# Kernel tuning notes

Measured on AMD Instinct MI355X. Metric: run time of the kernel, lower is better.

The kernel has to match this reference:

```python
import jax, jax.numpy as jnp
import numpy as np


def setup_inputs() -> dict:
    key = jax.random.key(0)
    ks = jax.random.split(key, 5)
    d_out, d_in = 4096, 4096
    r = min(d_out, d_in)
    B, T = 4, 2048
    x = jax.random.normal(ks[0], (B, T, d_in), dtype=jnp.float32)
    U = jax.random.normal(ks[1], (d_out, r), dtype=jnp.float32)
    S = jax.random.uniform(ks[2], (r,), dtype=jnp.float32)
    Vt = jax.random.normal(ks[3], (r, d_in), dtype=jnp.float32)
    epsilon = jnp.zeros((r,), dtype=jnp.float32)
    bias = jax.random.normal(ks[4], (d_out,), dtype=jnp.float32)
    return {"x": x, "U": U, "S": S, "Vt": Vt, "epsilon": epsilon, "bias": bias}


def reference(x, U, S, Vt, epsilon, bias):
    # w = U @ diag(S + epsilon) @ Vt  (diag folded as column scale of U)
    w = (U * (S + epsilon)[None, :]) @ Vt  # [d_out, d_in]
    # F.linear: y = x @ w.T + bias
    return jnp.einsum('btk,ok->bto', x, w) + bias
```

## Files before the change

### kernel.cpp

```cpp
#include <hip/hip_runtime.h>
#include <hip/hip_bf16.h>
#include <stdint.h>

typedef __attribute__((ext_vector_type(4))) float f32x4;
typedef __attribute__((ext_vector_type(8))) short short8v;

typedef __attribute__((address_space(1))) void gvoid;
typedef __attribute__((address_space(3))) void lvoid;

#define GLD16(gp, lp) __builtin_amdgcn_global_load_lds((const gvoid*)(gp), (lvoid*)(lp), 16, 0, 0)

__device__ __forceinline__ unsigned short f2bf(float f) {
    union { float ff; unsigned uu; } a; a.ff = f;
    unsigned u = a.uu;
    u += 0x7FFFu + ((u >> 16) & 1u);
    return (unsigned short)(u >> 16);
}

__global__ __launch_bounds__(256) void prep_fused_kernel(
    const float* __restrict__ U, const float* __restrict__ S,
    const float* __restrict__ eps, unsigned short* __restrict__ Ub,
    const float* __restrict__ Vt, unsigned short* __restrict__ VtT) {
    __shared__ float tile[64][65];
    if (blockIdx.x < 8192) {
        long idx = ((long)blockIdx.x * 256 + threadIdx.x) * 8;
        int r = (int)(idx & 4095);
        f32x4 u0 = *(const f32x4*)(U + idx);
        f32x4 u1 = *(const f32x4*)(U + idx + 4);
        f32x4 s0 = *(const f32x4*)(S + r);
        f32x4 s1 = *(const f32x4*)(S + r + 4);
        f32x4 e0 = *(const f32x4*)(eps + r);
        f32x4 e1 = *(const f32x4*)(eps + r + 4);
        union { uint4 v; unsigned short s[8]; } o;
#pragma unroll
        for (int j = 0; j < 4; ++j) {
            o.s[j]     = f2bf(u0[j] * (s0[j] + e0[j]));
            o.s[j + 4] = f2bf(u1[j] * (s1[j] + e1[j]));
        }
        *(uint4*)(Ub + idx) = o.v;
    } else {
        int t  = blockIdx.x - 8192;
        int k0 = (t & 63) << 6;
        int r0 = (t >> 6) << 6;
        int tx = threadIdx.x & 63;
        int tq = threadIdx.x >> 6;
#pragma unroll
        for (int i = 0; i < 16; ++i) {
            int row = (i << 2) + tq;
            tile[row][tx] = Vt[(long)(r0 + row) * 4096 + k0 + tx];
        }
        __syncthreads();
#pragma unroll
        for (int i = 0; i < 16; ++i) {
            int krow = (i << 2) + tq;
            VtT[(long)(k0 + krow) * 4096 + r0 + tx] = f2bf(tile[tx][krow]);
        }
    }
}

__global__ __launch_bounds__(256) void cvt_bf16_kernel(
    const float* __restrict__ src, unsigned short* __restrict__ dst) {
    long idx = ((long)blockIdx.x * 256 + threadIdx.x) * 8;
    f32x4 v0 = *(const f32x4*)(src + idx);
    f32x4 v1 = *(const f32x4*)(src + idx + 4);
    union { uint4 v; unsigned short s[8]; } o;
#pragma unroll
    for (int j = 0; j < 4; ++j) {
        o.s[j]     = f2bf(v0[j]);
        o.s[j + 4] = f2bf(v1[j]);
    }
    *(uint4*)(dst + idx) = o.v;
}

#define MM(a, b, c) __builtin_amdgcn_mfma_f32_16x16x32_bf16(a, b, c, 0, 0, 0)

#define ARG(r) (As + (r) * 8192)
#define BRG(r) (Bs + (r) * 8192)

#define STAGE_A(r, koff) do { \
    const unsigned short* _s = A + gAr + (koff); \
    unsigned short* _d = ARG(r) + wave * 512; \
    GLD16(_s, _d); GLD16(_s + (long)128 * K, _d + 4096); } while (0)

#define STAGE_B(r, koff) do { \
    const unsigned short* _s = B + gBr + (koff); \
    unsigned short* _d = BRG(r) + wave * 512; \
    GLD16(_s, _d); GLD16(_s + (long)128 * K, _d + 4096); } while (0)

#define DSR(dst, base, imm) \
    asm volatile("ds_read_b128 %0, %1 offset:%c2" \
                 : "=v"(dst) : "v"(base), "i"(imm))

#define READ_AB(bk, R) do { \
    DSR(aB[bk][0][0], aByte, (R)*16384 + 0);            \
    DSR(aB[bk][0][1], aByte, (R)*16384 + 1024);         \
    DSR(aB[bk][0][2], aByte, (R)*16384 + 2048);         \
    DSR(aB[bk][0][3], aByte, (R)*16384 + 3072);         \
    DSR(aB[bk][1][0], aByte, (R)*16384 + 4096);         \
    DSR(aB[bk][1][1], aByte, (R)*16384 + 5120);         \
    DSR(aB[bk][1][2], aByte, (R)*16384 + 6144);         \
    DSR(aB[bk][1][3], aByte, (R)*16384 + 7168);         \
    DSR(bB[bk][0],    bByte, (R)*16384 + 0);            \
    DSR(bB[bk][1],    bByte, (R)*16384 + 1024);         \
    DSR(bB[bk][2],    bByte, (R)*16384 + 2048);         \
    DSR(bB[bk][3],    bByte, (R)*16384 + 3072); } while (0)

#define MFMA32(bk) do { \
    _Pragma("unroll") \
    for (int _h = 0; _h < 2; ++_h) \
    _Pragma("unroll") \
    for (int _m = 0; _m < 4; ++_m) { \
        acc[_h*4+_m][0] = MM(aB[bk][_h][_m], bB[bk][0], acc[_h*4+_m][0]); \
        acc[_h*4+_m][1] = MM(aB[bk][_h][_m], bB[bk][1], acc[_h*4+_m][1]); \
        acc[_h*4+_m][2] = MM(aB[bk][_h][_m], bB[bk][2], acc[_h*4+_m][2]); \
        acc[_h*4+_m][3] = MM(aB[bk][_h][_m], bB[bk][3], acc[_h*4+_m][3]); \
    } } while (0)

#define SGB __builtin_amdgcn_sched_group_barrier

#define PHASE(rN, sb, rS, sk, cb) do { \
    STAGE_A(rS, sk); STAGE_B(rS, sk); \
    asm volatile("s_waitcnt lgkmcnt(0)" ::: "memory"); \
    __builtin_amdgcn_sched_barrier(0); \
    __builtin_amdgcn_s_setprio(1); \
    READ_AB(sb, rN); \
    MFMA32(cb); \
    _Pragma("unroll") \
    for (int _g = 0; _g < 12; ++_g) { SGB(0x008, 2, 0); SGB(0x100, 1, 0); } \
    SGB(0x008, 8, 0); \
    __builtin_amdgcn_s_setprio(0); \
    asm volatile("s_waitcnt vmcnt(4)" ::: "memory"); \
    __builtin_amdgcn_s_barrier(); } while (0)

template<int OUT_BF16, int BIAS>
__global__ __launch_bounds__(512, 2) void gemm256_kernel(
    const unsigned short* __restrict__ A,
    const unsigned short* __restrict__ B,
    void* __restrict__ Cv, const float* __restrict__ bias,
    int M, int N, int K) {
    __shared__ unsigned short As[4 * 8192];
    __shared__ unsigned short Bs[4 * 8192];

    const int tid  = threadIdx.x;
    const int wave = tid >> 6;
    const int lane = tid & 63;
    const int fr   = lane & 15;
    const int fq   = lane >> 4;

    const int nwg = gridDim.x;
    const int bid = blockIdx.x;
    const int cpx = nwg >> 3;
    const int wg  = (bid & 7) * cpx + (bid >> 3);
    const int nmt = M >> 8;
    const long n0 = (long)(2 * (wg / cpx) + (wg & 1)) << 8;
    const long m0 = (long)((wg >> 1) & (nmt - 1)) << 8;

    const int wwr = wave >> 2;
    const int wwc = wave & 3;

    const int  rS  = tid >> 2;
    const int  sS  = (tid & 3) ^ ((rS >> 1) & 3);
    const long gAr = (m0 + rS) * K + sS * 8;
    const long gBr = (n0 + rS) * K + sS * 8;

    const int swz   = (fq ^ ((fr >> 1) & 3)) * 8;
    const int aBase = (wwr * 128 + fr) * 32 + swz;
    const int bBase = (wwc * 64 + fr) * 32 + swz;
    const unsigned aByte = (unsigned)(uintptr_t)(As + aBase);
    const unsigned bByte = (unsigned)(uintptr_t)(Bs + bBase);

    f32x4  acc[8][4] = {};
    short8v aB[2][2][4], bB[2][4];

    STAGE_A(0, 0);  STAGE_B(0, 0);
    STAGE_A(1, 32); STAGE_B(1, 32);
    STAGE_A(2, 64); STAGE_B(2, 64);
    asm volatile("s_waitcnt vmcnt(4)" ::: "memory");
    __builtin_amdgcn_s_barrier();
    READ_AB(0, 0);

    const int nIter = K >> 7;
    for (int i = 0; i < nIter; ++i) {
        const int kA = 128 * i + 96;
        int k0n = 128 * i + 128; if (k0n >= K) k0n -= K;
        int k1n = 128 * i + 160; if (k1n >= K) k1n -= K;
        int k2n = 128 * i + 192; if (k2n >= K) k2n -= K;

        PHASE(1, 1, 3, kA,  0);
        PHASE(2, 0, 0, k0n, 1);
        PHASE(3, 1, 1, k1n, 0);
        PHASE(0, 0, 2, k2n, 1);
    }

#pragma unroll
    for (int nf = 0; nf < 4; ++nf) {
        const int col = (int)n0 + wwc * 64 + nf * 16 + fr;
        float bv = BIAS ? bias[col] : 0.0f;
#pragma unroll
        for (int mf = 0; mf < 8; ++mf) {
            f32x4 v = acc[mf][nf];
            long rowb = m0 + wwr * 128 + mf * 16 + fq * 4;
#pragma unroll
            for (int j = 0; j < 4; ++j) {
                float val = v[j] + bv;
                long off = (rowb + j) * N + col;
                if (OUT_BF16) ((unsigned short*)Cv)[off] = f2bf(val);
                else          ((float*)Cv)[off] = val;
            }
        }
    }
}

extern "C" void kernel_launch(void* const* d_in, const int* in_sizes, int n_in,
                              void* d_out, int out_size, void* d_ws, size_t ws_size,
                              hipStream_t stream) {
    const float* x    = (const float*)d_in[0];
    const float* U    = (const float*)d_in[1];
    const float* S    = (const float*)d_in[2];
    const float* Vt   = (const float*)d_in[3];
    const float* eps  = (const float*)d_in[4];
    const float* bias = (const float*)d_in[5];
    float* out = (float*)d_out;

    char* ws = (char*)d_ws;
    unsigned short* Ub  = (unsigned short*)(ws);
    unsigned short* VtT = (unsigned short*)(ws + (size_t)(32 << 20));
    unsigned short* Wb  = (unsigned short*)(ws + (size_t)(64 << 20));
    unsigned short* Xb  = (unsigned short*)(ws);

    prep_fused_kernel<<<12288, 256, 0, stream>>>(U, S, eps, Ub, Vt, VtT);
    gemm256_kernel<1, 0><<<256, 512, 0, stream>>>(Ub, VtT, (void*)Wb, nullptr,
                                                  4096, 4096, 4096);
    cvt_bf16_kernel<<<16384, 256, 0, stream>>>(x, Xb);
    gemm256_kernel<0, 1><<<512, 512, 0, stream>>>(Xb, Wb, (void*)out, bias,
                                                  8192, 4096, 4096);
}
```

Measured before the change: 433.6 us.

## Fuse x fp32-to-bf16 conversion into the weight-building GEMM main loop

Removes the separate conversion kernel for x and instead has each thread of the first GEMM load and convert a chunk of x once per K iteration. The conversion loads are interleaved with the LDS staging, with adjusted vmcnt waits, so they can hide behind MFMA work. This saves a kernel launch and lets the bandwidth-bound conversion overlap the compute-bound GEMM. In exchange it needs a larger workspace (falling back to the old path otherwise) and adds register and memory pressure to the GEMM pipeline.

```diff
diff --git a/kernel.cpp b/kernel.cpp
--- a/kernel.cpp
+++ b/kernel.cpp
@@ -118,6 +118,11 @@
 
 #define SGB __builtin_amdgcn_sched_group_barrier
 
+#define SGB_PATTERN do { \
+    _Pragma("unroll") \
+    for (int _g = 0; _g < 12; ++_g) { SGB(0x008, 2, 0); SGB(0x100, 1, 0); } \
+    SGB(0x008, 8, 0); } while (0)
+
 #define PHASE(rN, sb, rS, sk, cb) do { \
     STAGE_A(rS, sk); STAGE_B(rS, sk); \
     asm volatile("s_waitcnt lgkmcnt(0)" ::: "memory"); \
@@ -125,18 +130,26 @@
     __builtin_amdgcn_s_setprio(1); \
     READ_AB(sb, rN); \
     MFMA32(cb); \
-    _Pragma("unroll") \
-    for (int _g = 0; _g < 12; ++_g) { SGB(0x008, 2, 0); SGB(0x100, 1, 0); } \
-    SGB(0x008, 8, 0); \
+    SGB_PATTERN; \
     __builtin_amdgcn_s_setprio(0); \
     asm volatile("s_waitcnt vmcnt(4)" ::: "memory"); \
     __builtin_amdgcn_s_barrier(); } while (0)
 
-template<int OUT_BF16, int BIAS>
+#define XCVT_STORE do { \
+    union { uint4 v; unsigned short s[8]; } _o; \
+    _Pragma("unroll") \
+    for (int _j = 0; _j < 4; ++_j) { \
+        _o.s[_j]     = f2bf(xv0[_j]); \
+        _o.s[_j + 4] = f2bf(xv1[_j]); } \
+    *reinterpret_cast<uint4*>((uintptr_t)xsaddr) = _o.v; \
+    xsaddr += 2097152ull; } while (0)
+
+template<int OUT_BF16, int BIAS, int DO_CVT>
 __global__ __launch_bounds__(512, 2) void gemm256_kernel(
     const unsigned short* __restrict__ A,
     const unsigned short* __restrict__ B,
     void* __restrict__ Cv, const float* __restrict__ bias,
+    const float* __restrict__ xsrc, unsigned short* __restrict__ xdst,
     int M, int N, int K) {
     __shared__ unsigned short As[4 * 8192];
     __shared__ unsigned short Bs[4 * 8192];
@@ -172,6 +185,14 @@
     f32x4  acc[8][4] = {};
     short8v aB[2][2][4], bB[2][4];
 
+    f32x4 xv0, xv1;
+    unsigned long long xaddr = 0, xsaddr = 0;
+    if constexpr (DO_CVT) {
+        long gchunk = ((long)bid * 512 + tid);
+        xaddr  = (unsigned long long)(uintptr_t)(xsrc + gchunk * 8);
+        xsaddr = (unsigned long long)(uintptr_t)(xdst + gchunk * 8);
+    }
+
     STAGE_A(0, 0);  STAGE_B(0, 0);
     STAGE_A(1, 32); STAGE_B(1, 32);
     STAGE_A(2, 64); STAGE_B(2, 64);
@@ -186,11 +207,32 @@
         int k1n = 128 * i + 160; if (k1n >= K) k1n -= K;
         int k2n = 128 * i + 192; if (k2n >= K) k2n -= K;
 
-        PHASE(1, 1, 3, kA,  0);
+        if constexpr (DO_CVT) {
+            if (i) XCVT_STORE;
+            asm volatile("global_load_dwordx4 %0, %2, off\n\t"
+                         "global_load_dwordx4 %1, %2, off offset:16"
+                         : "=&v"(xv0), "=&v"(xv1) : "v"(xaddr));
+            xaddr += 4194304ull;
+            STAGE_A(3, kA); STAGE_B(3, kA);
+            asm volatile("s_waitcnt lgkmcnt(0)" ::: "memory");
+            __builtin_amdgcn_sched_barrier(0);
+            __builtin_amdgcn_s_setprio(1);
+            READ_AB(1, 1);
+            MFMA32(0);
+            SGB_PATTERN;
+            __builtin_amdgcn_s_setprio(0);
+            if (i) asm volatile("s_waitcnt vmcnt(7)" ::: "memory");
+            else   asm volatile("s_waitcnt vmcnt(6)" ::: "memory");
+            __builtin_amdgcn_s_barrier();
+        } else {
+            PHASE(1, 1, 3, kA,  0);
+        }
         PHASE(2, 0, 0, k0n, 1);
         PHASE(3, 1, 1, k1n, 0);
         PHASE(0, 0, 2, k2n, 1);
     }
+
+    if constexpr (DO_CVT) XCVT_STORE;
 
 #pragma unroll
     for (int nf = 0; nf < 4; ++nf) {
@@ -226,12 +268,21 @@
     unsigned short* Ub  = (unsigned short*)(ws);
     unsigned short* VtT = (unsigned short*)(ws + (size_t)(32 << 20));
     unsigned short* Wb  = (unsigned short*)(ws + (size_t)(64 << 20));
-    unsigned short* Xb  = (unsigned short*)(ws);
 
     prep_fused_kernel<<<12288, 256, 0, stream>>>(U, S, eps, Ub, Vt, VtT);
-    gemm256_kernel<1, 0><<<256, 512, 0, stream>>>(Ub, VtT, (void*)Wb, nullptr,
-                                                  4096, 4096, 4096);
-    cvt_bf16_kernel<<<16384, 256, 0, stream>>>(x, Xb);
-    gemm256_kernel<0, 1><<<512, 512, 0, stream>>>(Xb, Wb, (void*)out, bias,
-                                                  8192, 4096, 4096);
-}
+
+    if (ws_size >= ((size_t)160 << 20)) {
+        unsigned short* Xb = (unsigned short*)(ws + ((size_t)96 << 20));
+        gemm256_kernel<1, 0, 1><<<256, 512, 0, stream>>>(
+            Ub, VtT, (void*)Wb, nullptr, x, Xb, 4096, 4096, 4096);
+        gemm256_kernel<0, 1, 0><<<512, 512, 0, stream>>>(
+            Xb, Wb, (void*)out, bias, nullptr, nullptr, 8192, 4096, 4096);
+    } else {
+        unsigned short* Xb = (unsigned short*)(ws);
+        gemm256_kernel<1, 0, 0><<<256, 512, 0, stream>>>(
+            Ub, VtT, (void*)Wb, nullptr, nullptr, nullptr, 4096, 4096, 4096);
+        cvt_bf16_kernel<<<16384, 256, 0, stream>>>(x, Xb);
+        gemm256_kernel<0, 1, 0><<<512, 512, 0, stream>>>(
+            Xb, Wb, (void*)out, bias, nullptr, nullptr, 8192, 4096, 4096);
+    }
+}
```

After: 428.3 us (median of 3 runs). No clear change (-1.2%).

## Use 1024-thread GEMM tiles and fuse x bf16 conversion into first GEMM

Applied to the files above, without the earlier changes.

Moves the GEMM to 16 waves per 256x256 tile, so each wave computes 64x64 and holds 16 accumulators instead of 32. It drops the hand-scheduled double-buffered ds_read/MFMA interleave in favour of plain LDS loads and a simpler vmcnt(2) wait per phase. When the workspace is large enough, the first GEMM also converts x to bf16 inside its main loop, hiding the separate conversion kernel's memory traffic behind the W computation. The risks are losing the tuned instruction schedule and losing register-level reuse with smaller per-wave tiles.

```diff
diff --git a/kernel.cpp b/kernel.cpp
--- a/kernel.cpp
+++ b/kernel.cpp
@@ -77,66 +77,45 @@
 #define ARG(r) (As + (r) * 8192)
 #define BRG(r) (Bs + (r) * 8192)
 
-#define STAGE_A(r, koff) do { \
-    const unsigned short* _s = A + gAr + (koff); \
-    unsigned short* _d = ARG(r) + wave * 512; \
-    GLD16(_s, _d); GLD16(_s + (long)128 * K, _d + 4096); } while (0)
-
-#define STAGE_B(r, koff) do { \
-    const unsigned short* _s = B + gBr + (koff); \
-    unsigned short* _d = BRG(r) + wave * 512; \
-    GLD16(_s, _d); GLD16(_s + (long)128 * K, _d + 4096); } while (0)
-
-#define DSR(dst, base, imm) \
-    asm volatile("ds_read_b128 %0, %1 offset:%c2" \
-                 : "=v"(dst) : "v"(base), "i"(imm))
-
-#define READ_AB(bk, R) do { \
-    DSR(aB[bk][0][0], aByte, (R)*16384 + 0);            \
-    DSR(aB[bk][0][1], aByte, (R)*16384 + 1024);         \
-    DSR(aB[bk][0][2], aByte, (R)*16384 + 2048);         \
-    DSR(aB[bk][0][3], aByte, (R)*16384 + 3072);         \
-    DSR(aB[bk][1][0], aByte, (R)*16384 + 4096);         \
-    DSR(aB[bk][1][1], aByte, (R)*16384 + 5120);         \
-    DSR(aB[bk][1][2], aByte, (R)*16384 + 6144);         \
-    DSR(aB[bk][1][3], aByte, (R)*16384 + 7168);         \
-    DSR(bB[bk][0],    bByte, (R)*16384 + 0);            \
-    DSR(bB[bk][1],    bByte, (R)*16384 + 1024);         \
-    DSR(bB[bk][2],    bByte, (R)*16384 + 2048);         \
-    DSR(bB[bk][3],    bByte, (R)*16384 + 3072); } while (0)
-
-#define MFMA32(bk) do { \
+#define STAGE_A(r, koff) GLD16(A + gAr + (koff), ARG(r) + wave * 512)
+#define STAGE_B(r, koff) GLD16(B + gBr + (koff), BRG(r) + wave * 512)
+
+#define LOAD_A(r) do { \
+    const unsigned short* _p = ARG(r) + aBase; \
     _Pragma("unroll") \
-    for (int _h = 0; _h < 2; ++_h) \
+    for (int _m = 0; _m < 4; ++_m) aR[_m] = *(const short8v*)(_p + _m * 512); } while (0)
+
+#define READ_B(r) do { \
+    const unsigned short* _p = BRG(r) + bBase; \
+    _Pragma("unroll") \
+    for (int _n = 0; _n < 4; ++_n) bR[_n] = *(const short8v*)(_p + _n * 512); } while (0)
+
+#define MFMA16 do { \
+    __builtin_amdgcn_s_setprio(1); \
     _Pragma("unroll") \
     for (int _m = 0; _m < 4; ++_m) { \
-        acc[_h*4+_m][0] = MM(aB[bk][_h][_m], bB[bk][0], acc[_h*4+_m][0]); \
-        acc[_h*4+_m][1] = MM(aB[bk][_h][_m], bB[bk][1], acc[_h*4+_m][1]); \
-        acc[_h*4+_m][2] = MM(aB[bk][_h][_m], bB[bk][2], acc[_h*4+_m][2]); \
-        acc[_h*4+_m][3] = MM(aB[bk][_h][_m], bB[bk][3], acc[_h*4+_m][3]); \
-    } } while (0)
-
-#define SGB __builtin_amdgcn_sched_group_barrier
-
-#define PHASE(rN, sb, rS, sk, cb) do { \
-    STAGE_A(rS, sk); STAGE_B(rS, sk); \
-    asm volatile("s_waitcnt lgkmcnt(0)" ::: "memory"); \
-    __builtin_amdgcn_sched_barrier(0); \
-    __builtin_amdgcn_s_setprio(1); \
-    READ_AB(sb, rN); \
-    MFMA32(cb); \
-    _Pragma("unroll") \
-    for (int _g = 0; _g < 12; ++_g) { SGB(0x008, 2, 0); SGB(0x100, 1, 0); } \
-    SGB(0x008, 8, 0); \
-    __builtin_amdgcn_s_setprio(0); \
-    asm volatile("s_waitcnt vmcnt(4)" ::: "memory"); \
-    __builtin_amdgcn_s_barrier(); } while (0)
-
-template<int OUT_BF16, int BIAS>
-__global__ __launch_bounds__(512, 2) void gemm256_kernel(
+        acc[_m][0] = MM(aR[_m], bR[0], acc[_m][0]); \
+        acc[_m][1] = MM(aR[_m], bR[1], acc[_m][1]); \
+        acc[_m][2] = MM(aR[_m], bR[2], acc[_m][2]); \
+        acc[_m][3] = MM(aR[_m], bR[3], acc[_m][3]); \
+    } \
+    __builtin_amdgcn_s_setprio(0); } while (0)
+
+#define VM2 asm volatile("s_waitcnt vmcnt(2)" ::: "memory")
+#define BAR __builtin_amdgcn_s_barrier()
+
+#define PHASE(rd, st, sk) do { \
+    LOAD_A(rd); READ_B(rd); \
+    STAGE_A(st, sk); STAGE_B(st, sk); \
+    MFMA16; \
+    VM2; BAR; } while (0)
+
+template<int OUT_BF16, int BIAS, int DO_CVT>
+__global__ __launch_bounds__(1024, 4) void gemm256_kernel(
     const unsigned short* __restrict__ A,
     const unsigned short* __restrict__ B,
     void* __restrict__ Cv, const float* __restrict__ bias,
+    const float* __restrict__ xsrc, unsigned short* __restrict__ xdst,
     int M, int N, int K) {
     __shared__ unsigned short As[4 * 8192];
     __shared__ unsigned short Bs[4 * 8192];
@@ -164,20 +143,26 @@
     const long gBr = (n0 + rS) * K + sS * 8;
 
     const int swz   = (fq ^ ((fr >> 1) & 3)) * 8;
-    const int aBase = (wwr * 128 + fr) * 32 + swz;
+    const int aBase = (wwr * 64 + fr) * 32 + swz;
     const int bBase = (wwc * 64 + fr) * 32 + swz;
-    const unsigned aByte = (unsigned)(uintptr_t)(As + aBase);
-    const unsigned bByte = (unsigned)(uintptr_t)(Bs + bBase);
-
-    f32x4  acc[8][4] = {};
-    short8v aB[2][2][4], bB[2][4];
+
+    f32x4  acc[4][4] = {};
+    short8v aR[4], bR[4];
+
+    f32x4 xv;
+    unsigned long long xaddr = 0;
+    unsigned short* xs = nullptr;
+    if constexpr (DO_CVT) {
+        long base = (long)bid * 4096 + (long)tid * 4;
+        xaddr = (unsigned long long)(uintptr_t)(xsrc + base);
+        xs = xdst + base;
+    }
 
     STAGE_A(0, 0);  STAGE_B(0, 0);
     STAGE_A(1, 32); STAGE_B(1, 32);
     STAGE_A(2, 64); STAGE_B(2, 64);
-    asm volatile("s_waitcnt vmcnt(4)" ::: "memory");
-    __builtin_amdgcn_s_barrier();
-    READ_AB(0, 0);
+    VM2;
+    BAR;
 
     const int nIter = K >> 7;
     for (int i = 0; i < nIter; ++i) {
@@ -186,10 +171,34 @@
         int k1n = 128 * i + 160; if (k1n >= K) k1n -= K;
         int k2n = 128 * i + 192; if (k2n >= K) k2n -= K;
 
-        PHASE(1, 1, 3, kA,  0);
-        PHASE(2, 0, 0, k0n, 1);
-        PHASE(3, 1, 1, k1n, 0);
-        PHASE(0, 0, 2, k2n, 1);
+        if constexpr (DO_CVT) {
+            LOAD_A(0); READ_B(0);
+            if (i) {
+                union { unsigned uu[2]; unsigned short s[4]; } o;
+#pragma unroll
+                for (int j = 0; j < 4; ++j) o.s[j] = f2bf(xv[j]);
+                *(uint2*)xs = *(uint2*)o.uu;
+                xs += 1048576;
+            }
+            asm volatile("global_load_dwordx4 %0, %1, off"
+                         : "=v"(xv) : "v"(xaddr));
+            xaddr += 4194304ull;
+            STAGE_A(3, kA); STAGE_B(3, kA);
+            MFMA16;
+            VM2; BAR;
+        } else {
+            PHASE(0, 3, kA);
+        }
+        PHASE(1, 0, k0n);
+        PHASE(2, 1, k1n);
+        PHASE(3, 2, k2n);
+    }
+
+    if constexpr (DO_CVT) {
+        union { unsigned uu[2]; unsigned short s[4]; } o;
+#pragma unroll
+        for (int j = 0; j < 4; ++j) o.s[j] = f2bf(xv[j]);
+        *(uint2*)xs = *(uint2*)o.uu;
     }
 
 #pragma unroll
@@ -197,9 +206,9 @@
         const int col = (int)n0 + wwc * 64 + nf * 16 + fr;
         float bv = BIAS ? bias[col] : 0.0f;
 #pragma unroll
-        for (int mf = 0; mf < 8; ++mf) {
+        for (int mf = 0; mf < 4; ++mf) {
             f32x4 v = acc[mf][nf];
-            long rowb = m0 + wwr * 128 + mf * 16 + fq * 4;
+            long rowb = m0 + wwr * 64 + mf * 16 + fq * 4;
 #pragma unroll
             for (int j = 0; j < 4; ++j) {
                 float val = v[j] + bv;
@@ -226,12 +235,21 @@
     unsigned short* Ub  = (unsigned short*)(ws);
     unsigned short* VtT = (unsigned short*)(ws + (size_t)(32 << 20));
     unsigned short* Wb  = (unsigned short*)(ws + (size_t)(64 << 20));
-    unsigned short* Xb  = (unsigned short*)(ws);
 
     prep_fused_kernel<<<12288, 256, 0, stream>>>(U, S, eps, Ub, Vt, VtT);
-    gemm256_kernel<1, 0><<<256, 512, 0, stream>>>(Ub, VtT, (void*)Wb, nullptr,
-                                                  4096, 4096, 4096);
-    cvt_bf16_kernel<<<16384, 256, 0, stream>>>(x, Xb);
-    gemm256_kernel<0, 1><<<512, 512, 0, stream>>>(Xb, Wb, (void*)out, bias,
-                                                  8192, 4096, 4096);
-}
+
+    if (ws_size >= ((size_t)160 << 20)) {
+        unsigned short* Xb = (unsigned short*)(ws + ((size_t)96 << 20));
+        gemm256_kernel<1, 0, 1><<<256, 1024, 0, stream>>>(
+            Ub, VtT, (void*)Wb, nullptr, x, Xb, 4096, 4096, 4096);
+        gemm256_kernel<0, 1, 0><<<512, 1024, 0, stream>>>(
+            Xb, Wb, (void*)out, bias, nullptr, nullptr, 8192, 4096, 4096);
+    } else {
+        unsigned short* Xb = (unsigned short*)(ws);
+        gemm256_kernel<1, 0, 0><<<256, 1024, 0, stream>>>(
+            Ub, VtT, (void*)Wb, nullptr, nullptr, nullptr, 4096, 4096, 4096);
+        cvt_bf16_kernel<<<16384, 256, 0, stream>>>(x, Xb);
+        gemm256_kernel<0, 1, 0><<<512, 1024, 0, stream>>>(
+            Xb, Wb, (void*)out, bias, nullptr, nullptr, 8192, 4096, 4096);
+    }
+}
```

Measured after the change: 459.5 us. 6.0% more time.
